# Performance work log

Measured on AMD Instinct MI355X. Metric: run time of the kernel, lower is better.

Reference implementation:

```python
import jax, jax.numpy as jnp
import numpy as np
from jax import lax

N = 100000   # number of points / rows of X and inv[i]
C = 16       # input channels
F = 16       # filters
W = 8        # beam window width
D = 3        # dims (number of pre/post conv pairs)
NSEG = 8192  # number of beam segments (fixed stand-in for reduce_max(I)+1)


def _conv2d_relu(x, w, b):
    # x: [H, W, Cin], w: [kh, kw, Cin, Cout], 'same' padding + relu (keras Conv2D)
    y = lax.conv_general_dilated(x[None], w, (1, 1), 'SAME',
                                 dimension_numbers=('NHWC', 'HWIO', 'NHWC'))[0]
    return jax.nn.relu(y + b)


def setup_inputs() -> dict:
    key = jax.random.key(0)
    ks = jax.random.split(key, 5)
    X = jax.random.normal(ks[0], (N, C), jnp.float32)
    inv = jax.random.randint(ks[1], (D, N, W), 0, N, jnp.int32)
    index = jax.random.randint(ks[2], (D, N), 0, NSEG, jnp.int32)
    pre_w = jax.random.normal(ks[3], (D, 3, 3, C, F), jnp.float32) * 0.05
    pre_b = jnp.zeros((D, F), jnp.float32)
    post_w = jax.random.normal(ks[4], (D, 3, 1, F, F), jnp.float32) * 0.05
    post_b = jnp.zeros((D, F), jnp.float32)
    return {"X": X, "inv": inv, "index": index,
            "pre_w": pre_w, "pre_b": pre_b, "post_w": post_w, "post_b": post_b}


def reference(X, inv, index, pre_w, pre_b, post_w, post_b):
    Y = jnp.zeros((N, W, F), jnp.float32)
    for i in range(D):  # small fixed structural loop over dims
        x = X[inv[i]]                                      # gather_nd -> [N, W, C]
        x = _conv2d_relu(x, pre_w[i], pre_b[i])            # [N, W, F]
        I = index[i]                                       # [N] segment ids
        x = jax.ops.segment_sum(x, I, num_segments=NSEG)   # [NSEG, W, F]
        x = _conv2d_relu(x, post_w[i], post_b[i])          # (3,1) kernel, same pad
        Y = Y + x[I]                                       # gather back -> [N, W, F]
    return Y
```

## Files before the change

### kernel.cpp

```cpp
#include <hip/hip_runtime.h>

#define N_    100000
#define C_    16
#define F_    16
#define W_    8
#define D_    3
#define NSEG_ 8192
#define BR    16

#define SEGROW (W_*F_)
#define SEGBUF ((size_t)NSEG_ * SEGROW)

typedef __attribute__((ext_vector_type(4)))  float f32x4;
typedef __attribute__((ext_vector_type(8)))  short bf16x8;
typedef __attribute__((ext_vector_type(16))) short bf16x16;

static __device__ __forceinline__ short f2bf(float x) {
    union { float f; unsigned u; } v; v.f = x;
    unsigned r = v.u + 0x7fffu + ((v.u >> 16) & 1u);
    return (short)(r >> 16);
}

__global__ __launch_bounds__(256) void xprep_k(
    const float* __restrict__ X, short* __restrict__ Xbf)
{
    const int gid = blockIdx.x * 256 + threadIdx.x;
    if (gid >= (N_ * C_) / 8) return;
    const float4 v0 = *(const float4*)&X[(size_t)gid * 8];
    const float4 v1 = *(const float4*)&X[(size_t)gid * 8 + 4];
    bf16x8 o;
    o[0] = f2bf(v0.x); o[1] = f2bf(v0.y); o[2] = f2bf(v0.z); o[3] = f2bf(v0.w);
    o[4] = f2bf(v1.x); o[5] = f2bf(v1.y); o[6] = f2bf(v1.z); o[7] = f2bf(v1.w);
    *(bf16x8*)&Xbf[(size_t)gid * 8] = o;
}

__global__ __launch_bounds__(256) void wprep_k(
    const float* __restrict__ pre_w, short* __restrict__ wbT_g)
{
    const int k = blockIdx.x * 256 + threadIdx.x;
    const int i  = k / 2560;
    const int r  = k - i * 2560;
    const int f  = r / 160;
    const int kk = r - f * 160;
    wbT_g[k] = (kk < 144) ? f2bf(pre_w[i * 2304 + kk * 16 + f]) : (short)0;
}

__global__ __launch_bounds__(256) void preconv_seg_mfma(
    const short* __restrict__ Xbf, const int* __restrict__ inv,
    const int* __restrict__ index, const short* __restrict__ wbT_g,
    const float* __restrict__ pre_b, float* __restrict__ seg)
{
    const int i  = blockIdx.y;
    const int r0 = blockIdx.x * BR;
    const int t  = threadIdx.x;

    __shared__ __align__(32) short xg[20][10][16];
    __shared__ __align__(16) short wbT[16][160];
    __shared__ float bs[F_];
    __shared__ int   sidx[BR];

    int* xz = (int*)&xg[0][0][0];
    for (int k = t; k < 20 * 10 * 16 / 2; k += 256) xz[k] = 0;

    {
        const bf16x8* src = (const bf16x8*)(wbT_g + i * 2560);
        bf16x8* dst = (bf16x8*)&wbT[0][0];
        dst[t] = src[t];
        if (t < 64) dst[256 + t] = src[256 + t];
    }
    if (t < F_) bs[t] = pre_b[i * F_ + t];
    if (t < BR) sidx[t] = index[(size_t)i * N_ + r0 + t];
    __syncthreads();

    if (t < 144) {
        const int row = t >> 3, w = t & 7;
        const int n = r0 - 1 + row;
        if (n >= 0 && n < N_) {
            const int src = inv[((size_t)i * N_ + n) * W_ + w];
            *(bf16x16*)&xg[row][w + 1][0] =
                *(const bf16x16*)&Xbf[(size_t)src * C_];
        }
    }
    __syncthreads();

    const int lane = t & 63;
    const int wv   = t >> 6;
    const int fc   = lane & 15;
    const int kb   = lane >> 4;
    const int mA   = lane & 15;

#pragma unroll
    for (int tt = 0; tt < 2; ++tt) {
        const int m_base = (wv * 2 + tt) * 16;
        const int m  = m_base + mA;
        const int nl = m >> 3;
        const int w  = m & 7;
        f32x4 acc = {0.f, 0.f, 0.f, 0.f};
#pragma unroll
        for (int s = 0; s < 5; ++s) {
            const int g  = s * 4 + kb;
            const int gg = g >> 1;
            const int c0 = (g & 1) * 8;
            const int dr = gg / 3;
            const int dw = gg - dr * 3;
            const bf16x8 a = *(const bf16x8*)&xg[nl + dr][w + dw][c0];
            const bf16x8 b = *(const bf16x8*)&wbT[fc][s * 32 + kb * 8];
            acc = __builtin_amdgcn_mfma_f32_16x16x32_bf16(a, b, acc, 0, 0, 0);
        }
#pragma unroll
        for (int r = 0; r < 4; ++r) {
            const int mc  = m_base + kb * 4 + r;
            const int nlc = mc >> 3, wc = mc & 7;
            const float v = fmaxf(acc[r] + bs[fc], 0.f);
            atomicAdd(&seg[((size_t)i * NSEG_ + sidx[nlc]) * SEGROW + wc * F_ + fc], v);
        }
    }
}

__global__ __launch_bounds__(256) void postconv(
    const float* __restrict__ seg, const float* __restrict__ post_w,
    const float* __restrict__ post_b, float* __restrict__ post)
{
    const int i = blockIdx.y;
    const int t = threadIdx.x;

    __shared__ float ws[3][F_][F_];
    __shared__ float bs[F_];
    for (int k = t; k < 3 * F_ * F_; k += 256)
        (&ws[0][0][0])[k] = post_w[i * 3 * F_ * F_ + k];
    if (t < F_) bs[t] = post_b[i * F_ + t];
    __syncthreads();

    const int idx = blockIdx.x * 256 + t;
    const int fo  = idx & 15;
    const int w   = (idx >> 4) & 7;
    const int s   = idx >> 7;

    float acc = bs[fo];
#pragma unroll
    for (int dh = 0; dh < 3; ++dh) {
        const int ss = s + dh - 1;
        if (ss < 0 || ss >= NSEG_) continue;
        const float* sp = seg + ((size_t)i * NSEG_ + ss) * SEGROW + w * F_;
        const float4 s0 = *(const float4*)(sp);
        const float4 s1 = *(const float4*)(sp + 4);
        const float4 s2 = *(const float4*)(sp + 8);
        const float4 s3 = *(const float4*)(sp + 12);
        const float sv[16] = {s0.x, s0.y, s0.z, s0.w, s1.x, s1.y, s1.z, s1.w,
                              s2.x, s2.y, s2.z, s2.w, s3.x, s3.y, s3.z, s3.w};
#pragma unroll
        for (int fi = 0; fi < F_; ++fi)
            acc += sv[fi] * ws[dh][fi][fo];
    }
    post[(size_t)i * SEGBUF + idx] = fmaxf(acc, 0.f);
}

__global__ __launch_bounds__(256) void gather_sum(
    const float* __restrict__ post, const int* __restrict__ index,
    float* __restrict__ Y)
{
    const int gt = blockIdx.x * 256 + threadIdx.x;
    if (gt >= N_ * 32) return;
    const int q = gt & 31;
    const int n = gt >> 5;

    float4 acc = make_float4(0.f, 0.f, 0.f, 0.f);
#pragma unroll
    for (int i = 0; i < D_; ++i) {
        const int s = index[(size_t)i * N_ + n];
        const float4 v = *(const float4*)&post[(size_t)i * SEGBUF +
                                               (size_t)s * SEGROW + q * 4];
        acc.x += v.x; acc.y += v.y; acc.z += v.z; acc.w += v.w;
    }
    *(float4*)&Y[(size_t)n * SEGROW + q * 4] = acc;
}

extern "C" void kernel_launch(void* const* d_in, const int* in_sizes, int n_in,
                              void* d_out, int out_size, void* d_ws, size_t ws_size,
                              hipStream_t stream)
{
    const float* X      = (const float*)d_in[0];
    const int*   inv    = (const int*)  d_in[1];
    const int*   index  = (const int*)  d_in[2];
    const float* pre_w  = (const float*)d_in[3];
    const float* pre_b  = (const float*)d_in[4];
    const float* post_w = (const float*)d_in[5];
    const float* post_b = (const float*)d_in[6];
    float*       Y      = (float*)d_out;

    char* p = (char*)d_ws;
    float* seg   = (float*)p;   p += D_ * SEGBUF * sizeof(float);
    float* post  = (float*)p;   p += D_ * SEGBUF * sizeof(float);
    short* Xbf   = (short*)p;   p += (size_t)N_ * C_ * sizeof(short);
    short* wbT_g = (short*)p;   p += D_ * F_ * 160 * sizeof(short);

    hipMemsetAsync(seg, 0, D_ * SEGBUF * sizeof(float), stream);

    xprep_k<<<(N_ * C_ / 8 + 255) / 256, 256, 0, stream>>>(X, Xbf);
    wprep_k<<<30, 256, 0, stream>>>(pre_w, wbT_g);

    preconv_seg_mfma<<<dim3(N_ / BR, D_), 256, 0, stream>>>(
        Xbf, inv, index, wbT_g, pre_b, seg);

    postconv<<<dim3((NSEG_ * W_ * F_) / 256, D_), 256, 0, stream>>>(
        seg, post_w, post_b, post);
    gather_sum<<<dim3((N_ * 32 + 255) / 256), 256, 0, stream>>>(post, index, Y);
}
```

Baseline: 263.8 us.

## Accumulate segment sums with packed bf16 atomics into two split buffers

Switches the scatter-add segment buffer from fp32 atomics to packed bf16 atomics (global_atomic_pk_add_bf16), which halves the number of atomic operations and the bytes moved. Even and odd row blocks write to two separate copies of the buffer to cut contention, and postconv adds the two copies together when it reads them. The cost is lower accumulation precision, since bf16 atomic adds over many contributions can drift from the fp32 reference. It also relies on inline assembly for the atomic.

```diff
diff --git a/kernel.cpp b/kernel.cpp
--- a/kernel.cpp
+++ b/kernel.cpp
@@ -19,6 +19,11 @@
     union { float f; unsigned u; } v; v.f = x;
     unsigned r = v.u + 0x7fffu + ((v.u >> 16) & 1u);
     return (short)(r >> 16);
+}
+static __device__ __forceinline__ float bf2f(short x) {
+    union { unsigned u; float f; } c;
+    c.u = ((unsigned)(unsigned short)x) << 16;
+    return c.f;
 }
 
 __global__ __launch_bounds__(256) void xprep_k(
@@ -48,11 +53,12 @@
 __global__ __launch_bounds__(256) void preconv_seg_mfma(
     const short* __restrict__ Xbf, const int* __restrict__ inv,
     const int* __restrict__ index, const short* __restrict__ wbT_g,
-    const float* __restrict__ pre_b, float* __restrict__ seg)
+    const float* __restrict__ pre_b, short* __restrict__ seg)
 {
     const int i  = blockIdx.y;
     const int r0 = blockIdx.x * BR;
     const int t  = threadIdx.x;
+    const size_t half_off = (size_t)(blockIdx.x & 1) * (D_ * SEGBUF);
 
     __shared__ __align__(32) short xg[20][10][16];
     __shared__ __align__(16) short wbT[16][160];
@@ -111,14 +117,24 @@
         for (int r = 0; r < 4; ++r) {
             const int mc  = m_base + kb * 4 + r;
             const int nlc = mc >> 3, wc = mc & 7;
-            const float v = fmaxf(acc[r] + bs[fc], 0.f);
-            atomicAdd(&seg[((size_t)i * NSEG_ + sidx[nlc]) * SEGROW + wc * F_ + fc], v);
+            const float v  = fmaxf(acc[r] + bs[fc], 0.f);
+            const float vx = __shfl_xor(v, 1);
+            if (!(fc & 1)) {
+                const unsigned lo = (unsigned)(unsigned short)f2bf(v);
+                const unsigned hi = (unsigned)(unsigned short)f2bf(vx);
+                const unsigned packed = (hi << 16) | lo;
+                const short* addr = seg + half_off +
+                    ((size_t)i * NSEG_ + sidx[nlc]) * SEGROW + wc * F_ + fc;
+                asm volatile("global_atomic_pk_add_bf16 %0, %1, off"
+                             :: "v"((unsigned long long)(uintptr_t)addr),
+                                "v"(packed) : "memory");
+            }
         }
     }
 }
 
 __global__ __launch_bounds__(256) void postconv(
-    const float* __restrict__ seg, const float* __restrict__ post_w,
+    const short* __restrict__ seg, const float* __restrict__ post_w,
     const float* __restrict__ post_b, float* __restrict__ post)
 {
     const int i = blockIdx.y;
@@ -141,13 +157,13 @@
     for (int dh = 0; dh < 3; ++dh) {
         const int ss = s + dh - 1;
         if (ss < 0 || ss >= NSEG_) continue;
-        const float* sp = seg + ((size_t)i * NSEG_ + ss) * SEGROW + w * F_;
-        const float4 s0 = *(const float4*)(sp);
-        const float4 s1 = *(const float4*)(sp + 4);
-        const float4 s2 = *(const float4*)(sp + 8);
-        const float4 s3 = *(const float4*)(sp + 12);
-        const float sv[16] = {s0.x, s0.y, s0.z, s0.w, s1.x, s1.y, s1.z, s1.w,
-                              s2.x, s2.y, s2.z, s2.w, s3.x, s3.y, s3.z, s3.w};
+        const short* sp0 = seg + ((size_t)i * NSEG_ + ss) * SEGROW + w * F_;
+        const short* sp1 = sp0 + D_ * SEGBUF;
+        const bf16x16 a = *(const bf16x16*)sp0;
+        const bf16x16 b = *(const bf16x16*)sp1;
+        float sv[16];
+#pragma unroll
+        for (int fi = 0; fi < 16; ++fi) sv[fi] = bf2f(a[fi]) + bf2f(b[fi]);
 #pragma unroll
         for (int fi = 0; fi < F_; ++fi)
             acc += sv[fi] * ws[dh][fi][fo];
@@ -189,12 +205,12 @@
     float*       Y      = (float*)d_out;
 
     char* p = (char*)d_ws;
-    float* seg   = (float*)p;   p += D_ * SEGBUF * sizeof(float);
+    short* seg   = (short*)p;   p += 2 * D_ * SEGBUF * sizeof(short);
     float* post  = (float*)p;   p += D_ * SEGBUF * sizeof(float);
     short* Xbf   = (short*)p;   p += (size_t)N_ * C_ * sizeof(short);
     short* wbT_g = (short*)p;   p += D_ * F_ * 160 * sizeof(short);
 
-    hipMemsetAsync(seg, 0, D_ * SEGBUF * sizeof(float), stream);
+    hipMemsetAsync(seg, 0, 2 * D_ * SEGBUF * sizeof(short), stream);
 
     xprep_k<<<(N_ * C_ / 8 + 255) / 256, 256, 0, stream>>>(X, Xbf);
     wprep_k<<<30, 256, 0, stream>>>(pre_w, wbT_g);
```

New measurement: 272.3 us. +3.2%, slower.
